# Performance work log

Measured on AMD Instinct MI355X. Metric: run time of the kernel, lower is better.

## Reference

```python
import jax, jax.numpy as jnp
import numpy as np

B, S, D, U = 4, 2048, 1024, 1024

def setup_inputs() -> dict:
    key = jax.random.key(0)
    ks = jax.random.split(key, 6)
    glorot = lambda k, shape: jax.random.uniform(k, shape, jnp.float32,
                                                 -np.sqrt(6.0/(shape[0]+shape[1])),
                                                 np.sqrt(6.0/(shape[0]+shape[1])))
    return {
        "inputs": jax.random.normal(ks[0], (B, S, D), jnp.float32),
        "Wq": glorot(ks[1], (D, U)),
        "Wk": glorot(ks[2], (D, U)),
        "Wv": glorot(ks[3], (D, U)),
        "Wo": glorot(ks[4], (U, D)),
        "bo": jnp.zeros((D,), jnp.float32),
        "scale": jnp.asarray(1.0 / np.sqrt(U), jnp.float32),
    }

def reference(inputs, Wq, Wk, Wv, Wo, bo, scale):
    # q, k, v: [B, S, U]
    q = jnp.einsum('bsd,du->bsu', inputs, Wq)
    k = jnp.einsum('bsd,du->bsu', inputs, Wk)
    v = jnp.einsum('bsd,du->bsu', inputs, Wv)
    # scores: [B, S, S]
    scores = jnp.einsum('bqu,bku->bqk', q, k) * scale
    weights = jax.nn.softmax(scores, axis=-1)
    context = jnp.einsum('bqk,bku->bqu', weights, v)
    output = jnp.einsum('bsu,ud->bsd', context, Wo) + bo
    return (output, weights)
```

## Files before the change

kernel.cpp:

```cpp
#include <hip/hip_runtime.h>
#include <hip/hip_bf16.h>

#define BB 4
#define SS 2048
#define DD 1024
#define UU 1024
#define NTOK (BB*SS)

typedef unsigned short ushort_t;
typedef __attribute__((ext_vector_type(8))) short bf16x8;
typedef __attribute__((ext_vector_type(4))) float f32x4;
typedef __attribute__((ext_vector_type(4))) unsigned short u16x4;

__device__ inline unsigned short f2bf(float f) {
  unsigned u = __builtin_bit_cast(unsigned, f);
  u += 0x7FFFu + ((u >> 16) & 1u);
  return (unsigned short)(u >> 16);
}

__device__ inline void gload_lds16(const ushort_t* g, ushort_t* l) {
  __builtin_amdgcn_global_load_lds(
      (const __attribute__((address_space(1))) void*)g,
      (__attribute__((address_space(3))) void*)l, 16, 0, 0);
}

#define WAIT_LGKM0 do { asm volatile("s_waitcnt lgkmcnt(0)" ::: "memory"); \
                        __builtin_amdgcn_sched_barrier(0); } while(0)
#define WAIT_VM0   do { asm volatile("s_waitcnt vmcnt(0)" ::: "memory"); \
                        __builtin_amdgcn_sched_barrier(0); } while(0)
#define BAR        do { __builtin_amdgcn_s_barrier(); \
                        __builtin_amdgcn_sched_barrier(0); } while(0)

__global__ __launch_bounds__(256) void cast_f32_bf16(const float* __restrict__ in,
                                                     ushort_t* __restrict__ out,
                                                     long n) {
  long i = ((long)blockIdx.x * blockDim.x + threadIdx.x) * 4;
  long stride = (long)gridDim.x * blockDim.x * 4;
  for (long idx = i; idx < n; idx += stride) {
    float4 v = *(const float4*)(in + idx);
    u16x4 o;
    o[0] = f2bf(v.x); o[1] = f2bf(v.y); o[2] = f2bf(v.z); o[3] = f2bf(v.w);
    *(u16x4*)(out + idx) = o;
  }
}

__global__ __launch_bounds__(256) void transpose_cast_w(const float* __restrict__ in,
                                                        ushort_t* __restrict__ out,
                                                        int R, int C) {
  __shared__ float tile[32][33];
  int bx = blockIdx.x * 32, by = blockIdx.y * 32;
  int tx = threadIdx.x, ty = threadIdx.y;
  #pragma unroll
  for (int j = 0; j < 32; j += 8)
    tile[ty + j][tx] = in[(long)(by + ty + j) * C + bx + tx];
  __syncthreads();
  #pragma unroll
  for (int j = 0; j < 32; j += 8)
    out[(long)(bx + ty + j) * R + by + tx] = f2bf(tile[tx][ty + j]);
}

__global__ __launch_bounds__(256) void transpose_bf16_batched(const ushort_t* __restrict__ in,
                                                              ushort_t* __restrict__ out,
                                                              int R, int C) {
  __shared__ ushort_t tile[32][34];
  long z = (long)blockIdx.z * R * C;
  int bx = blockIdx.x * 32, by = blockIdx.y * 32;
  int tx = threadIdx.x, ty = threadIdx.y;
  #pragma unroll
  for (int j = 0; j < 32; j += 8)
    tile[ty + j][tx] = in[z + (long)(by + ty + j) * C + bx + tx];
  __syncthreads();
  #pragma unroll
  for (int j = 0; j < 32; j += 8)
    out[z + (long)(bx + ty + j) * R + by + tx] = tile[tx][ty + j];
}

template<int BN>
__global__ __launch_bounds__(512, 2) void gemm8p(
    const ushort_t* __restrict__ A,
    const ushort_t* __restrict__ Bt,
    float* __restrict__ Cf,
    ushort_t* __restrict__ Cb,
    const float* __restrict__ bias,
    const float* __restrict__ alpha_ptr,
    int M, int N, int K,
    long sA, long sB, long sC) {
  static_assert(BN == 128 || BN == 256, "BN");
  constexpr int NREP = BN / 64;
  constexpr int BSTEPS = BN / 64;
  __shared__ __align__(16) ushort_t As[2][256 * 64];
  __shared__ __align__(16) ushort_t Bs[2][BN * 64];

  const int tid = threadIdx.x;
  const int lane = tid & 63;
  const int wid = tid >> 6;
  const int wm = wid >> 2, wn = wid & 3;
  const long zA = (long)blockIdx.z * sA;
  const long zB = (long)blockIdx.z * sB;
  const long zC = (long)blockIdx.z * sC;
  const int m0 = blockIdx.y * 256;
  const int n0 = blockIdx.x * BN;

  f32x4 acc[8][NREP] = {};

  const int srow = tid >> 3;
  const int cs = (tid & 7) ^ (srow & 7);
  const ushort_t* Aps = A + zA + (long)(m0 + srow) * K + cs * 8;
  const ushort_t* Bps = Bt + zB + (long)(n0 + srow) * K + cs * 8;
  const int ldst = (wid * 64) * 8;

  const int rsel = (lane & 15);
  const int csel = (lane >> 4);
  const int cxor = (lane & 7);

  const int nt = K / 64;

  #pragma unroll
  for (int j = 0; j < 4; ++j)
    gload_lds16(Aps + (long)(j * 64) * K, &As[0][j * 4096 + ldst]);
  #pragma unroll
  for (int j = 0; j < BSTEPS; ++j)
    gload_lds16(Bps + (long)(j * 64) * K, &Bs[0][j * 4096 + ldst]);
  WAIT_VM0;
  BAR;

  for (int t = 0; t < nt; ++t) {
    const int cur = t & 1, nxt = cur ^ 1;
    const int k1 = (t + 1) * 64;
    const bool pf = (t + 1 < nt);
    const ushort_t* __restrict__ Ac = &As[cur][0];
    const ushort_t* __restrict__ Bc = &Bs[cur][0];

    bf16x8 bfr[NREP][2], af[4][2];

    #pragma unroll
    for (int n = 0; n < NREP; ++n)
      #pragma unroll
      for (int kk = 0; kk < 2; ++kk)
        bfr[n][kk] = *(const bf16x8*)&Bc[(wn * (BN/4) + n * 16 + rsel) * 64
                                         + ((kk * 4 + csel) ^ cxor) * 8];
    #pragma unroll
    for (int m = 0; m < 4; ++m)
      #pragma unroll
      for (int kk = 0; kk < 2; ++kk)
        af[m][kk] = *(const bf16x8*)&Ac[(wm * 128 + m * 16 + rsel) * 64
                                        + ((kk * 4 + csel) ^ cxor) * 8];
    if (pf) {
      gload_lds16(Aps + (long)(0 * 64) * K + k1, &As[nxt][0 * 4096 + ldst]);
      gload_lds16(Aps + (long)(1 * 64) * K + k1, &As[nxt][1 * 4096 + ldst]);
      gload_lds16(Bps + (long)(0 * 64) * K + k1, &Bs[nxt][0 * 4096 + ldst]);
      if (BN == 256)
        gload_lds16(Bps + (long)(1 * 64) * K + k1, &Bs[nxt][1 * 4096 + ldst]);
    }
    BAR;
    WAIT_LGKM0;
    __builtin_amdgcn_s_setprio(1);
    #pragma unroll
    for (int m = 0; m < 4; ++m)
      #pragma unroll
      for (int n = 0; n < (NREP == 4 ? 2 : NREP); ++n)
        #pragma unroll
        for (int kk = 0; kk < 2; ++kk)
          acc[m][n] = __builtin_amdgcn_mfma_f32_16x16x32_bf16(af[m][kk], bfr[n][kk], acc[m][n], 0, 0, 0);
    __builtin_amdgcn_s_setprio(0);
    BAR;

    if (NREP == 4) {
      if (pf) {
        gload_lds16(Aps + (long)(2 * 64) * K + k1, &As[nxt][2 * 4096 + ldst]);
        gload_lds16(Aps + (long)(3 * 64) * K + k1, &As[nxt][3 * 4096 + ldst]);
        gload_lds16(Bps + (long)(2 * 64) * K + k1, &Bs[nxt][2 * 4096 + ldst]);
        gload_lds16(Bps + (long)(3 * 64) * K + k1, &Bs[nxt][3 * 4096 + ldst]);
      }
      BAR;
      __builtin_amdgcn_s_setprio(1);
      #pragma unroll
      for (int m = 0; m < 4; ++m)
        #pragma unroll
        for (int n = 2; n < 4; ++n)
          #pragma unroll
          for (int kk = 0; kk < 2; ++kk)
            acc[m][n] = __builtin_amdgcn_mfma_f32_16x16x32_bf16(af[m][kk], bfr[n][kk], acc[m][n], 0, 0, 0);
      __builtin_amdgcn_s_setprio(0);
      BAR;

      #pragma unroll
      for (int m = 0; m < 4; ++m)
        #pragma unroll
        for (int kk = 0; kk < 2; ++kk)
          af[m][kk] = *(const bf16x8*)&Ac[(wm * 128 + 64 + m * 16 + rsel) * 64
                                          + ((kk * 4 + csel) ^ cxor) * 8];
      BAR;
      WAIT_LGKM0;
      __builtin_amdgcn_s_setprio(1);
      #pragma unroll
      for (int m = 0; m < 4; ++m)
        #pragma unroll
        for (int n = 0; n < 2; ++n)
          #pragma unroll
          for (int kk = 0; kk < 2; ++kk)
            acc[m + 4][n] = __builtin_amdgcn_mfma_f32_16x16x32_bf16(af[m][kk], bfr[n][kk], acc[m + 4][n], 0, 0, 0);
      __builtin_amdgcn_s_setprio(0);
      BAR;

      __builtin_amdgcn_s_setprio(1);
      #pragma unroll
      for (int m = 0; m < 4; ++m)
        #pragma unroll
        for (int n = 2; n < 4; ++n)
          #pragma unroll
          for (int kk = 0; kk < 2; ++kk)
            acc[m + 4][n] = __builtin_amdgcn_mfma_f32_16x16x32_bf16(af[m][kk], bfr[n][kk], acc[m + 4][n], 0, 0, 0);
      __builtin_amdgcn_s_setprio(0);
    } else {
      #pragma unroll
      for (int m = 0; m < 4; ++m)
        #pragma unroll
        for (int kk = 0; kk < 2; ++kk)
          af[m][kk] = *(const bf16x8*)&Ac[(wm * 128 + 64 + m * 16 + rsel) * 64
                                          + ((kk * 4 + csel) ^ cxor) * 8];
      if (pf) {
        gload_lds16(Aps + (long)(2 * 64) * K + k1, &As[nxt][2 * 4096 + ldst]);
        gload_lds16(Aps + (long)(3 * 64) * K + k1, &As[nxt][3 * 4096 + ldst]);
        gload_lds16(Bps + (long)(1 * 64) * K + k1, &Bs[nxt][1 * 4096 + ldst]);
      }
      BAR;
      WAIT_LGKM0;
      __builtin_amdgcn_s_setprio(1);
      #pragma unroll
      for (int m = 0; m < 4; ++m)
        #pragma unroll
        for (int n = 0; n < NREP; ++n)
          #pragma unroll
          for (int kk = 0; kk < 2; ++kk)
            acc[m + 4][n] = __builtin_amdgcn_mfma_f32_16x16x32_bf16(af[m][kk], bfr[n][kk], acc[m + 4][n], 0, 0, 0);
      __builtin_amdgcn_s_setprio(0);
    }

    WAIT_VM0;
    BAR;
  }

  const float alpha = alpha_ptr ? *alpha_ptr : 1.0f;
  const int crow0 = m0 + wm * 128 + csel * 4;
  const int ccol0 = n0 + wn * (BN / 4) + rsel;
  #pragma unroll
  for (int m = 0; m < 8; ++m) {
    #pragma unroll
    for (int n = 0; n < NREP; ++n) {
      const int cc = ccol0 + n * 16;
      const float bv = bias ? bias[cc] : 0.0f;
      #pragma unroll
      for (int r = 0; r < 4; ++r) {
        const int rr = crow0 + m * 16 + r;
        const float v = acc[m][n][r] * alpha + bv;
        const long idx = zC + (long)rr * N + cc;
        if (Cf) Cf[idx] = v;
        if (Cb) Cb[idx] = f2bf(v);
      }
    }
  }
}

__global__ __launch_bounds__(256) void softmax_rows(float* __restrict__ Wf,
                                                    ushort_t* __restrict__ Pb) {
  const int t = threadIdx.x;
  const int lane = t & 63, wid = t >> 6;
  const long base = (long)blockIdx.x * SS;
  float* p = Wf + base;

  float4 a = *(const float4*)(p + t * 4);
  float4 b = *(const float4*)(p + 1024 + t * 4);

  float m = fmaxf(fmaxf(fmaxf(a.x, a.y), fmaxf(a.z, a.w)),
                  fmaxf(fmaxf(b.x, b.y), fmaxf(b.z, b.w)));
  #pragma unroll
  for (int off = 32; off; off >>= 1) m = fmaxf(m, __shfl_xor(m, off));
  __shared__ float redm[4];
  __shared__ float reds[4];
  if (lane == 0) redm[wid] = m;
  __syncthreads();
  m = fmaxf(fmaxf(redm[0], redm[1]), fmaxf(redm[2], redm[3]));

  float e[8];
  e[0] = __expf(a.x - m); e[1] = __expf(a.y - m); e[2] = __expf(a.z - m); e[3] = __expf(a.w - m);
  e[4] = __expf(b.x - m); e[5] = __expf(b.y - m); e[6] = __expf(b.z - m); e[7] = __expf(b.w - m);
  float s = (e[0] + e[1]) + (e[2] + e[3]) + (e[4] + e[5]) + (e[6] + e[7]);
  #pragma unroll
  for (int off = 32; off; off >>= 1) s += __shfl_xor(s, off);
  if (lane == 0) reds[wid] = s;
  __syncthreads();
  s = (reds[0] + reds[1]) + (reds[2] + reds[3]);
  const float inv = 1.0f / s;

  float4 oa = make_float4(e[0] * inv, e[1] * inv, e[2] * inv, e[3] * inv);
  float4 ob = make_float4(e[4] * inv, e[5] * inv, e[6] * inv, e[7] * inv);
  *(float4*)(p + t * 4) = oa;
  *(float4*)(p + 1024 + t * 4) = ob;

  u16x4 ba, bb2;
  ba[0] = f2bf(oa.x); ba[1] = f2bf(oa.y); ba[2] = f2bf(oa.z); ba[3] = f2bf(oa.w);
  bb2[0] = f2bf(ob.x); bb2[1] = f2bf(ob.y); bb2[2] = f2bf(ob.z); bb2[3] = f2bf(ob.w);
  *(u16x4*)(Pb + base + t * 4) = ba;
  *(u16x4*)(Pb + base + 1024 + t * 4) = bb2;
}

extern "C" void kernel_launch(void* const* d_in, const int* in_sizes, int n_in,
                              void* d_out, int out_size, void* d_ws, size_t ws_size,
                              hipStream_t stream) {
  const float* X     = (const float*)d_in[0];
  const float* Wq    = (const float*)d_in[1];
  const float* Wk    = (const float*)d_in[2];
  const float* Wv    = (const float*)d_in[3];
  const float* Wo    = (const float*)d_in[4];
  const float* bo    = (const float*)d_in[5];
  const float* scale = (const float*)d_in[6];

  float* out = (float*)d_out;
  float* wts = out + (long)NTOK * DD;

  ushort_t* ws = (ushort_t*)d_ws;
  ushort_t* Xb  = ws;
  ushort_t* Qb  = Xb + (long)NTOK * DD;
  ushort_t* Kb  = Qb + (long)NTOK * UU;
  ushort_t* Vb  = Kb + (long)NTOK * UU;
  ushort_t* Wqt = Vb + (long)NTOK * UU;
  ushort_t* Wkt = Wqt + (long)UU * DD;
  ushort_t* Wvt = Wkt + (long)UU * DD;
  ushort_t* Wot = Wvt + (long)UU * DD;
  ushort_t* Cb  = Xb;
  ushort_t* Vt  = Qb;
  ushort_t* Pb  = Kb;

  cast_f32_bf16<<<2048, 256, 0, stream>>>(X, Xb, (long)NTOK * DD);

  transpose_cast_w<<<dim3(UU/32, DD/32), dim3(32, 8), 0, stream>>>(Wq, Wqt, DD, UU);
  transpose_cast_w<<<dim3(UU/32, DD/32), dim3(32, 8), 0, stream>>>(Wk, Wkt, DD, UU);
  transpose_cast_w<<<dim3(UU/32, DD/32), dim3(32, 8), 0, stream>>>(Wv, Wvt, DD, UU);
  transpose_cast_w<<<dim3(DD/32, UU/32), dim3(32, 8), 0, stream>>>(Wo, Wot, UU, DD);

  dim3 gProj(UU/128, NTOK/256, 1);
  gemm8p<128><<<gProj, 512, 0, stream>>>(Xb, Wqt, nullptr, Qb, nullptr, nullptr,
                                         NTOK, UU, DD, 0, 0, 0);
  gemm8p<128><<<gProj, 512, 0, stream>>>(Xb, Wkt, nullptr, Kb, nullptr, nullptr,
                                         NTOK, UU, DD, 0, 0, 0);
  gemm8p<128><<<gProj, 512, 0, stream>>>(Xb, Wvt, nullptr, Vb, nullptr, nullptr,
                                         NTOK, UU, DD, 0, 0, 0);

  dim3 gScores(SS/256, SS/256, BB);
  gemm8p<256><<<gScores, 512, 0, stream>>>(Qb, Kb, wts, nullptr, nullptr, scale,
                                           SS, SS, UU,
                                           (long)SS * UU, (long)SS * UU, (long)SS * SS);

  transpose_bf16_batched<<<dim3(UU/32, SS/32, BB), dim3(32, 8), 0, stream>>>(Vb, Vt, SS, UU);

  softmax_rows<<<BB * SS, 256, 0, stream>>>(wts, Pb);

  dim3 gPV(UU/128, SS/256, BB);
  gemm8p<128><<<gPV, 512, 0, stream>>>(Pb, Vt, nullptr, Cb, nullptr, nullptr,
                                       SS, UU, SS,
                                       (long)SS * SS, (long)UU * SS, (long)SS * UU);

  dim3 gOut(DD/128, NTOK/256, 1);
  gemm8p<128><<<gOut, 512, 0, stream>>>(Cb, Wot, out, nullptr, bo, nullptr,
                                        NTOK, DD, UU, 0, 0, 0);
}
```

Before: 379.6 us.

## Issue full-stage prefetch early with partial vmcnt waits, XCD-aware block remap, batch launches

The GEMM now issues the whole next K-tile prefetch at the start of each iteration and uses partial vmcnt waits, so compute on earlier tiles overlaps the remaining loads. This replaces the full drain at the end of every iteration. Block indices are remapped so that consecutive tiles land on the same XCD, aiming for better L2 reuse. The four weight transposes are merged into one launch and the Q/K/V projections into one batched launch via blockIdx.z. The partial-wait counts must exactly match the load order, otherwise reads could race.

Measured after the change: 361.1 us. 1.05x faster.

```diff
diff --git a/kernel.cpp b/kernel.cpp
--- a/kernel.cpp
+++ b/kernel.cpp
@@ -26,7 +26,7 @@
 
 #define WAIT_LGKM0 do { asm volatile("s_waitcnt lgkmcnt(0)" ::: "memory"); \
                         __builtin_amdgcn_sched_barrier(0); } while(0)
-#define WAIT_VM0   do { asm volatile("s_waitcnt vmcnt(0)" ::: "memory"); \
+#define WAIT_VM(N) do { asm volatile("s_waitcnt vmcnt(" #N ")" ::: "memory"); \
                         __builtin_amdgcn_sched_barrier(0); } while(0)
 #define BAR        do { __builtin_amdgcn_s_barrier(); \
                         __builtin_amdgcn_sched_barrier(0); } while(0)
@@ -44,19 +44,20 @@
   }
 }
 
-__global__ __launch_bounds__(256) void transpose_cast_w(const float* __restrict__ in,
-                                                        ushort_t* __restrict__ out,
-                                                        int R, int C) {
+struct TPack { const float* s[4]; ushort_t* d[4]; };
+__global__ __launch_bounds__(256) void transpose_cast_w4(TPack p) {
   __shared__ float tile[32][33];
+  const float* in = p.s[blockIdx.z];
+  ushort_t* out = p.d[blockIdx.z];
   int bx = blockIdx.x * 32, by = blockIdx.y * 32;
   int tx = threadIdx.x, ty = threadIdx.y;
   #pragma unroll
   for (int j = 0; j < 32; j += 8)
-    tile[ty + j][tx] = in[(long)(by + ty + j) * C + bx + tx];
+    tile[ty + j][tx] = in[(long)(by + ty + j) * 1024 + bx + tx];
   __syncthreads();
   #pragma unroll
   for (int j = 0; j < 32; j += 8)
-    out[(long)(bx + ty + j) * R + by + tx] = f2bf(tile[tx][ty + j]);
+    out[(long)(bx + ty + j) * 1024 + by + tx] = f2bf(tile[tx][ty + j]);
 }
 
 __global__ __launch_bounds__(256) void transpose_bf16_batched(const ushort_t* __restrict__ in,
@@ -95,11 +96,25 @@
   const int lane = tid & 63;
   const int wid = tid >> 6;
   const int wm = wid >> 2, wn = wid & 3;
-  const long zA = (long)blockIdx.z * sA;
-  const long zB = (long)blockIdx.z * sB;
-  const long zC = (long)blockIdx.z * sC;
-  const int m0 = blockIdx.y * 256;
-  const int n0 = blockIdx.x * BN;
+
+  int bx = blockIdx.x, by = blockIdx.y, bz = blockIdx.z;
+  {
+    const int gx = gridDim.x, gy = gridDim.y, gz = gridDim.z;
+    const int total = gx * gy * gz;
+    const int ppx = total >> 3;
+    if ((total & 7) == 0 && ppx % gx == 0) {
+      const int lin = blockIdx.x + gx * (blockIdx.y + gy * blockIdx.z);
+      const int xcd = lin & 7, i = lin >> 3;
+      const int p = xcd * (ppx / gx) + i / gx;
+      bx = i % gx; by = p % gy; bz = p / gy;
+    }
+  }
+
+  const long zA = (long)bz * sA;
+  const long zB = (long)bz * sB;
+  const long zC = (long)bz * sC;
+  const int m0 = by * 256;
+  const int n0 = bx * BN;
 
   f32x4 acc[8][NREP] = {};
 
@@ -107,7 +122,7 @@
   const int cs = (tid & 7) ^ (srow & 7);
   const ushort_t* Aps = A + zA + (long)(m0 + srow) * K + cs * 8;
   const ushort_t* Bps = Bt + zB + (long)(n0 + srow) * K + cs * 8;
-  const int ldst = (wid * 64) * 8;
+  const int ldst = wid * 512;
 
   const int rsel = (lane & 15);
   const int csel = (lane >> 4);
@@ -115,18 +130,23 @@
 
   const int nt = K / 64;
 
-  #pragma unroll
-  for (int j = 0; j < 4; ++j)
-    gload_lds16(Aps + (long)(j * 64) * K, &As[0][j * 4096 + ldst]);
-  #pragma unroll
-  for (int j = 0; j < BSTEPS; ++j)
-    gload_lds16(Bps + (long)(j * 64) * K, &Bs[0][j * 4096 + ldst]);
-  WAIT_VM0;
+  auto STAGE = [&](int tk, int b) {
+    const long kof = (long)tk * 64;
+    #pragma unroll
+    for (int j = 0; j < BSTEPS; ++j)
+      gload_lds16(Bps + (long)(j * 64) * K + kof, &Bs[b][j * 4096 + ldst]);
+    gload_lds16(Aps + (long)(0 * 64) * K + kof, &As[b][0 * 4096 + ldst]);
+    gload_lds16(Aps + (long)(2 * 64) * K + kof, &As[b][2 * 4096 + ldst]);
+    gload_lds16(Aps + (long)(1 * 64) * K + kof, &As[b][1 * 4096 + ldst]);
+    gload_lds16(Aps + (long)(3 * 64) * K + kof, &As[b][3 * 4096 + ldst]);
+  };
+
+  STAGE(0, 0);
+  WAIT_VM(2);
   BAR;
 
   for (int t = 0; t < nt; ++t) {
     const int cur = t & 1, nxt = cur ^ 1;
-    const int k1 = (t + 1) * 64;
     const bool pf = (t + 1 < nt);
     const ushort_t* __restrict__ Ac = &As[cur][0];
     const ushort_t* __restrict__ Bc = &Bs[cur][0];
@@ -145,13 +165,7 @@
       for (int kk = 0; kk < 2; ++kk)
         af[m][kk] = *(const bf16x8*)&Ac[(wm * 128 + m * 16 + rsel) * 64
                                         + ((kk * 4 + csel) ^ cxor) * 8];
-    if (pf) {
-      gload_lds16(Aps + (long)(0 * 64) * K + k1, &As[nxt][0 * 4096 + ldst]);
-      gload_lds16(Aps + (long)(1 * 64) * K + k1, &As[nxt][1 * 4096 + ldst]);
-      gload_lds16(Bps + (long)(0 * 64) * K + k1, &Bs[nxt][0 * 4096 + ldst]);
-      if (BN == 256)
-        gload_lds16(Bps + (long)(1 * 64) * K + k1, &Bs[nxt][1 * 4096 + ldst]);
-    }
+    if (pf) STAGE(t + 1, nxt);
     BAR;
     WAIT_LGKM0;
     __builtin_amdgcn_s_setprio(1);
@@ -166,13 +180,6 @@
     BAR;
 
     if (NREP == 4) {
-      if (pf) {
-        gload_lds16(Aps + (long)(2 * 64) * K + k1, &As[nxt][2 * 4096 + ldst]);
-        gload_lds16(Aps + (long)(3 * 64) * K + k1, &As[nxt][3 * 4096 + ldst]);
-        gload_lds16(Bps + (long)(2 * 64) * K + k1, &Bs[nxt][2 * 4096 + ldst]);
-        gload_lds16(Bps + (long)(3 * 64) * K + k1, &Bs[nxt][3 * 4096 + ldst]);
-      }
-      BAR;
       __builtin_amdgcn_s_setprio(1);
       #pragma unroll
       for (int m = 0; m < 4; ++m)
@@ -182,6 +189,7 @@
           for (int kk = 0; kk < 2; ++kk)
             acc[m][n] = __builtin_amdgcn_mfma_f32_16x16x32_bf16(af[m][kk], bfr[n][kk], acc[m][n], 0, 0, 0);
       __builtin_amdgcn_s_setprio(0);
+      if (pf) { WAIT_VM(8); } else { WAIT_VM(0); }
       BAR;
 
       #pragma unroll
@@ -212,18 +220,18 @@
           for (int kk = 0; kk < 2; ++kk)
             acc[m + 4][n] = __builtin_amdgcn_mfma_f32_16x16x32_bf16(af[m][kk], bfr[n][kk], acc[m + 4][n], 0, 0, 0);
       __builtin_amdgcn_s_setprio(0);
+      if (pf) { WAIT_VM(2); }
+      BAR;
     } else {
+      if (pf) { WAIT_VM(6); } else { WAIT_VM(0); }
+      BAR;
+
       #pragma unroll
       for (int m = 0; m < 4; ++m)
         #pragma unroll
         for (int kk = 0; kk < 2; ++kk)
           af[m][kk] = *(const bf16x8*)&Ac[(wm * 128 + 64 + m * 16 + rsel) * 64
                                           + ((kk * 4 + csel) ^ cxor) * 8];
-      if (pf) {
-        gload_lds16(Aps + (long)(2 * 64) * K + k1, &As[nxt][2 * 4096 + ldst]);
-        gload_lds16(Aps + (long)(3 * 64) * K + k1, &As[nxt][3 * 4096 + ldst]);
-        gload_lds16(Bps + (long)(1 * 64) * K + k1, &Bs[nxt][1 * 4096 + ldst]);
-      }
       BAR;
       WAIT_LGKM0;
       __builtin_amdgcn_s_setprio(1);
@@ -235,10 +243,9 @@
           for (int kk = 0; kk < 2; ++kk)
             acc[m + 4][n] = __builtin_amdgcn_mfma_f32_16x16x32_bf16(af[m][kk], bfr[n][kk], acc[m + 4][n], 0, 0, 0);
       __builtin_amdgcn_s_setprio(0);
+      if (pf) { WAIT_VM(2); }
+      BAR;
     }
-
-    WAIT_VM0;
-    BAR;
   }
 
   const float alpha = alpha_ptr ? *alpha_ptr : 1.0f;
@@ -334,18 +341,15 @@
 
   cast_f32_bf16<<<2048, 256, 0, stream>>>(X, Xb, (long)NTOK * DD);
 
-  transpose_cast_w<<<dim3(UU/32, DD/32), dim3(32, 8), 0, stream>>>(Wq, Wqt, DD, UU);
-  transpose_cast_w<<<dim3(UU/32, DD/32), dim3(32, 8), 0, stream>>>(Wk, Wkt, DD, UU);
-  transpose_cast_w<<<dim3(UU/32, DD/32), dim3(32, 8), 0, stream>>>(Wv, Wvt, DD, UU);
-  transpose_cast_w<<<dim3(DD/32, UU/32), dim3(32, 8), 0, stream>>>(Wo, Wot, UU, DD);
-
-  dim3 gProj(UU/128, NTOK/256, 1);
+  TPack tp;
+  tp.s[0] = Wq; tp.s[1] = Wk; tp.s[2] = Wv; tp.s[3] = Wo;
+  tp.d[0] = Wqt; tp.d[1] = Wkt; tp.d[2] = Wvt; tp.d[3] = Wot;
+  transpose_cast_w4<<<dim3(32, 32, 4), dim3(32, 8), 0, stream>>>(tp);
+
+  dim3 gProj(UU/128, NTOK/256, 3);
   gemm8p<128><<<gProj, 512, 0, stream>>>(Xb, Wqt, nullptr, Qb, nullptr, nullptr,
-                                         NTOK, UU, DD, 0, 0, 0);
-  gemm8p<128><<<gProj, 512, 0, stream>>>(Xb, Wkt, nullptr, Kb, nullptr, nullptr,
-                                         NTOK, UU, DD, 0, 0, 0);
-  gemm8p<128><<<gProj, 512, 0, stream>>>(Xb, Wvt, nullptr, Vb, nullptr, nullptr,
-                                         NTOK, UU, DD, 0, 0, 0);
+                                         NTOK, UU, DD,
+                                         0, (long)UU * DD, (long)NTOK * UU);
 
   dim3 gScores(SS/256, SS/256, BB);
   gemm8p<256><<<gScores, 512, 0, stream>>>(Qb, Kb, wts, nullptr, nullptr, scale,
```
